# Kernel optimization log

Measured on AMD Instinct MI355X. Metric: run time of the kernel, lower is better.

The kernel has to match this reference:

```python
import jax, jax.numpy as jnp
import numpy as np

N_NODES = 100000


def setup_inputs() -> dict:
    key = jax.random.key(0)
    k1, k2, k3 = jax.random.split(key, 3)
    x = jax.random.normal(k1, (N_NODES, 64), dtype=jnp.float32)
    edge_index = jax.random.randint(k2, (2, 1250000), 0, N_NODES, dtype=jnp.int64)
    W = jax.random.normal(k3, (128, 64), dtype=jnp.float32) * (1.0 / np.sqrt(128.0))
    b = jnp.zeros((64,), dtype=jnp.float32)
    return {"x": x, "edge_index": edge_index, "W": W, "b": b}


def reference(x, edge_index, W, b):
    n = x.shape[0]
    row, col = edge_index[0], edge_index[1]
    # scatter-add neighbor features onto destination nodes
    neigh = jax.ops.segment_sum(x[row], col, num_segments=n)          # [n, d]
    count = jax.ops.segment_sum(jnp.ones_like(col, dtype=x.dtype), col, num_segments=n)
    count = jnp.where(count == 0, jnp.asarray(1.0, x.dtype), count)   # avoid div-by-zero
    neigh = neigh / count[:, None]                                    # mean aggregation
    x_aggr = jnp.concatenate([x, neigh], axis=-1)                     # [n, 2d]
    out = x_aggr @ W + b                                              # [n, out_dim]
    return jax.nn.relu(out)  # dropout=0.0 (eval) -> identity
```

## Files before the change

kernel.cpp:

```cpp
#include <hip/hip_runtime.h>

#define D 64
#define NPB 64
#define THREADS 512
#define CAP 64
#define NFILLB 1792
#define NCONVB 256

typedef int v4i __attribute__((ext_vector_type(4)));
typedef short bf16x8 __attribute__((ext_vector_type(8)));
typedef float f32x4 __attribute__((ext_vector_type(4)));

__device__ __forceinline__ unsigned short f2bf(float f) {
  unsigned u = __float_as_uint(f);
  return (unsigned short)((u + 0x7FFFu + ((u >> 16) & 1u)) >> 16);
}
__device__ __forceinline__ float bf2f(unsigned short h) {
  return __uint_as_float(((unsigned)h) << 16);
}
__device__ __forceinline__ void bfsplit(float v, unsigned short& hi, unsigned short& lo) {
  unsigned u = __float_as_uint(v);
  hi = (unsigned short)(u >> 16);
  float r = v - __uint_as_float(u & 0xFFFF0000u);
  lo = f2bf(r);
}

__global__ __launch_bounds__(256, 8) void fill_prep_kernel(
    const int* __restrict__ ei, int* __restrict__ cnt,
    int* __restrict__ bucket, int e, int qpc,
    const float* __restrict__ x, ushort* __restrict__ xh,
    const float* __restrict__ W, ushort* __restrict__ wth,
    ushort* __restrict__ wtl, int n, int total4) {
  if (blockIdx.x < NFILLB) {
    const int myx = blockIdx.x & 7;
    const int chunk = blockIdx.x >> 3;
    const int quads = e >> 2;
    const v4i* row4 = (const v4i*)ei;
    const v4i* col4 = (const v4i*)(ei + e);
    int qend = chunk * qpc + qpc;
    if (qend > quads) qend = quads;
    for (int q = chunk * qpc + threadIdx.x; q < qend; q += 256) {
      v4i r = __builtin_nontemporal_load(&row4[q]);
      v4i c = __builtin_nontemporal_load(&col4[q]);
      if (((c.x >> 11) & 7) == myx) {
        int p = atomicAdd(&cnt[c.x], 1);
        if (p < CAP) bucket[(size_t)c.x * CAP + p] = r.x * D;
      }
      if (((c.y >> 11) & 7) == myx) {
        int p = atomicAdd(&cnt[c.y], 1);
        if (p < CAP) bucket[(size_t)c.y * CAP + p] = r.y * D;
      }
      if (((c.z >> 11) & 7) == myx) {
        int p = atomicAdd(&cnt[c.z], 1);
        if (p < CAP) bucket[(size_t)c.z * CAP + p] = r.z * D;
      }
      if (((c.w >> 11) & 7) == myx) {
        int p = atomicAdd(&cnt[c.w], 1);
        if (p < CAP) bucket[(size_t)c.w * CAP + p] = r.w * D;
      }
    }
  } else {
    int t = (blockIdx.x - NFILLB) * 256 + threadIdx.x;
    int nth = NCONVB * 256;
    for (int i = t; i < 2 * D * D; i += nth) {
      int nn = i >> 7, k = i & 127;
      float v = W[k * D + nn];
      unsigned short hi, lo;
      bfsplit(v, hi, lo);
      wth[i] = hi;
      wtl[i] = lo;
    }
    for (int i = t; i < total4; i += nth) {
      float4 v = ((const float4*)x)[i];
      ushort4 h;
      h.x = f2bf(v.x); h.y = f2bf(v.y); h.z = f2bf(v.z); h.w = f2bf(v.w);
      ((ushort4*)xh)[i] = h;
    }
  }
}

__global__ __launch_bounds__(THREADS, 8) void fused_bf_kernel(
    const float* __restrict__ x, const ushort* __restrict__ xh,
    const int* __restrict__ cnt,
    const ushort* __restrict__ wth, const ushort* __restrict__ wtl,
    const float* __restrict__ b, float* __restrict__ out, int n) {
  __shared__ __align__(16) ushort xsh[NPB * 128];
  __shared__ __align__(16) ushort xsl[NPB * 128];

  const int lane = threadIdx.x & 63;
  const int wid  = threadIdx.x >> 6;
  const int base = blockIdx.x * NPB;
  const int* bucket = (const int*)out;
  const ushort* xpl = xh + lane;

  for (int m = 0; m < 8; ++m) {
    int nl = wid * 8 + m;
    int node = base + nl;
    int koff = nl * 128;
    int k0 = lane ^ ((nl & 7) << 3);
    if (node < n) {
      int dg = cnt[node];
      int dc = dg < CAP ? dg : CAP;
      int bk = bucket[(size_t)node * CAP + lane];
      float xown = x[(size_t)node * D + lane];
      float s0 = 0.f, s1 = 0.f, s2 = 0.f, s3 = 0.f;
      float s4 = 0.f, s5 = 0.f, s6 = 0.f, s7 = 0.f;
      int p = 0;
      for (; p + 8 <= dc; p += 8) {
        int a0 = __shfl(bk, p),     a1 = __shfl(bk, p + 1);
        int a2 = __shfl(bk, p + 2), a3 = __shfl(bk, p + 3);
        int a4 = __shfl(bk, p + 4), a5 = __shfl(bk, p + 5);
        int a6 = __shfl(bk, p + 6), a7 = __shfl(bk, p + 7);
        s0 += bf2f(xpl[a0]); s1 += bf2f(xpl[a1]);
        s2 += bf2f(xpl[a2]); s3 += bf2f(xpl[a3]);
        s4 += bf2f(xpl[a4]); s5 += bf2f(xpl[a5]);
        s6 += bf2f(xpl[a6]); s7 += bf2f(xpl[a7]);
      }
      for (; p + 4 <= dc; p += 4) {
        int a0 = __shfl(bk, p),     a1 = __shfl(bk, p + 1);
        int a2 = __shfl(bk, p + 2), a3 = __shfl(bk, p + 3);
        s0 += bf2f(xpl[a0]); s1 += bf2f(xpl[a1]);
        s2 += bf2f(xpl[a2]); s3 += bf2f(xpl[a3]);
      }
      for (; p < dc; ++p)
        s0 += bf2f(xpl[__shfl(bk, p)]);
      float sum = ((s0 + s1) + (s2 + s3)) + ((s4 + s5) + (s6 + s7));
      float inv = (dg > 0) ? (1.0f / (float)dg) : 0.0f;
      float mean = sum * inv;
      unsigned short h, l;
      bfsplit(xown, h, l);
      xsh[koff + k0] = h;       xsl[koff + k0] = l;
      bfsplit(mean, h, l);
      xsh[koff + 64 + k0] = h;  xsl[koff + 64 + k0] = l;
    } else {
      xsh[koff + k0] = 0;       xsl[koff + k0] = 0;
      xsh[koff + 64 + k0] = 0;  xsl[koff + 64 + k0] = 0;
    }
  }
  __syncthreads();

  const int mt   = wid >> 1;
  const int nb   = (wid & 1) * 32;
  const int lrow = lane & 15;
  const int kgrp = (lane >> 4) * 8;

  const int arow = mt * 16 + lrow;
  const int aswz = (arow & 7) << 3;
  const int abase = arow * 128;

  const ushort* wh0 = wth + (nb + lrow) * 128;
  const ushort* wh1 = wth + (nb + 16 + lrow) * 128;
  const ushort* wl0 = wtl + (nb + lrow) * 128;
  const ushort* wl1 = wtl + (nb + 16 + lrow) * 128;

  float bias0 = b[nb + lrow];
  float bias1 = b[nb + 16 + lrow];
  f32x4 acc0 = {bias0, bias0, bias0, bias0};
  f32x4 acc1 = {bias1, bias1, bias1, bias1};

#pragma unroll 2
  for (int ks = 0; ks < 4; ++ks) {
    int kb = ks * 32 + kgrp;
    int ke = abase + (kb ^ aswz);
    bf16x8 ah = *(const bf16x8*)&xsh[ke];
    bf16x8 al = *(const bf16x8*)&xsl[ke];
    bf16x8 w0h = *(const bf16x8*)(wh0 + kb);
    bf16x8 w1h = *(const bf16x8*)(wh1 + kb);
    acc0 = __builtin_amdgcn_mfma_f32_16x16x32_bf16(ah, w0h, acc0, 0, 0, 0);
    acc1 = __builtin_amdgcn_mfma_f32_16x16x32_bf16(ah, w1h, acc1, 0, 0, 0);
    acc0 = __builtin_amdgcn_mfma_f32_16x16x32_bf16(al, w0h, acc0, 0, 0, 0);
    acc1 = __builtin_amdgcn_mfma_f32_16x16x32_bf16(al, w1h, acc1, 0, 0, 0);
    bf16x8 w0l = *(const bf16x8*)(wl0 + kb);
    bf16x8 w1l = *(const bf16x8*)(wl1 + kb);
    acc0 = __builtin_amdgcn_mfma_f32_16x16x32_bf16(ah, w0l, acc0, 0, 0, 0);
    acc1 = __builtin_amdgcn_mfma_f32_16x16x32_bf16(ah, w1l, acc1, 0, 0, 0);
  }

  const int drow = (lane >> 4) * 4;
#pragma unroll
  for (int r = 0; r < 4; ++r) {
    int node = base + mt * 16 + drow + r;
    if (node < n) {
      out[(size_t)node * D + nb + lrow]      = fmaxf(acc0[r], 0.0f);
      out[(size_t)node * D + nb + 16 + lrow] = fmaxf(acc1[r], 0.0f);
    }
  }
}

__global__ __launch_bounds__(256) void fill_cap_kernel(
    const int* __restrict__ ei, int* __restrict__ cnt,
    int* __restrict__ bucket, int e) {
  int t = blockIdx.x * blockDim.x + threadIdx.x;
  if (t * 4 >= e) return;
  int4 r4 = ((const int4*)ei)[t];
  int4 c4 = ((const int4*)(ei + e))[t];
  int p0 = atomicAdd(&cnt[c4.x], 1);
  int p1 = atomicAdd(&cnt[c4.y], 1);
  int p2 = atomicAdd(&cnt[c4.z], 1);
  int p3 = atomicAdd(&cnt[c4.w], 1);
  if (p0 < CAP) bucket[(size_t)c4.x * CAP + p0] = r4.x;
  if (p1 < CAP) bucket[(size_t)c4.y * CAP + p1] = r4.y;
  if (p2 < CAP) bucket[(size_t)c4.z * CAP + p2] = r4.z;
  if (p3 < CAP) bucket[(size_t)c4.w * CAP + p3] = r4.w;
}

__global__ __launch_bounds__(THREADS, 8) void fused_cap_kernel(
    const float* __restrict__ x, const int* __restrict__ cnt,
    const float* __restrict__ W, const float* __restrict__ b,
    float* __restrict__ out, int n) {
  __shared__ __align__(16) float xs[NPB * 128];
  const int lane = threadIdx.x & 63;
  const int wid  = threadIdx.x >> 6;
  const int base = blockIdx.x * NPB;
  const int* bucket = (const int*)out;

  for (int m = 0; m < 8; ++m) {
    int nl = wid * 8 + m;
    int node = base + nl;
    if (node < n) {
      int dg = cnt[node];
      int dc = dg < CAP ? dg : CAP;
      int bk = bucket[(size_t)node * CAP + lane];
      float xown = x[(size_t)node * D + lane];
      float s0 = 0.f, s1 = 0.f, s2 = 0.f, s3 = 0.f;
      int p = 0;
      for (; p + 4 <= dc; p += 4) {
        int a0 = __shfl(bk, p),     a1 = __shfl(bk, p + 1);
        int a2 = __shfl(bk, p + 2), a3 = __shfl(bk, p + 3);
        s0 += x[(size_t)a0 * D + lane];
        s1 += x[(size_t)a1 * D + lane];
        s2 += x[(size_t)a2 * D + lane];
        s3 += x[(size_t)a3 * D + lane];
      }
      for (; p < dc; ++p)
        s0 += x[(size_t)__shfl(bk, p) * D + lane];
      float sum = (s0 + s1) + (s2 + s3);
      float inv = (dg > 0) ? (1.0f / (float)dg) : 0.0f;
      xs[nl * 128 + lane]      = xown;
      xs[nl * 128 + 64 + lane] = sum * inv;
    } else {
      xs[nl * 128 + lane]      = 0.0f;
      xs[nl * 128 + 64 + lane] = 0.0f;
    }
  }
  __syncthreads();

  const int col = lane;
  float bias = b[col];
  float acc[8];
#pragma unroll
  for (int m = 0; m < 8; ++m) acc[m] = bias;
  for (int k = 0; k < 128; k += 4) {
    float w0 = W[(k + 0) * 64 + col];
    float w1 = W[(k + 1) * 64 + col];
    float w2 = W[(k + 2) * 64 + col];
    float w3 = W[(k + 3) * 64 + col];
#pragma unroll
    for (int m = 0; m < 8; ++m) {
      int nl = wid + m * 8;
      float4 xv = *(const float4*)&xs[nl * 128 + k];
      acc[m] = fmaf(xv.x, w0, acc[m]);
      acc[m] = fmaf(xv.y, w1, acc[m]);
      acc[m] = fmaf(xv.z, w2, acc[m]);
      acc[m] = fmaf(xv.w, w3, acc[m]);
    }
  }
#pragma unroll
  for (int m = 0; m < 8; ++m) {
    int node = base + wid + m * 8;
    if (node < n)
      out[(size_t)node * D + col] = fmaxf(acc[m], 0.0f);
  }
}

extern "C" void kernel_launch(void* const* d_in, const int* in_sizes, int n_in,
                              void* d_out, int out_size, void* d_ws, size_t ws_size,
                              hipStream_t stream) {
  const float* x = (const float*)d_in[0];
  const int* ei = (const int*)d_in[1];
  const float* W = (const float*)d_in[2];
  const float* b = (const float*)d_in[3];
  float* out = (float*)d_out;

  int n = in_sizes[0] / D;
  int e = in_sizes[1] / 2;
  int nblocks = (n + NPB - 1) / NPB;

  size_t xh_bytes = (size_t)n * D * sizeof(ushort);
  size_t cnt_off  = (xh_bytes + 255) & ~(size_t)255;
  size_t wth_off  = (cnt_off + (size_t)n * sizeof(int) + 255) & ~(size_t)255;
  size_t wtl_off  = wth_off + 2 * D * D * sizeof(ushort);
  size_t need     = wtl_off + 2 * D * D * sizeof(ushort) + 256;

  if (ws_size >= need && (e & 3) == 0 && n <= (1 << 17)) {
    ushort* xh   = (ushort*)d_ws;
    int* cnt     = (int*)((char*)d_ws + cnt_off);
    ushort* wth  = (ushort*)((char*)d_ws + wth_off);
    ushort* wtl  = (ushort*)((char*)d_ws + wtl_off);

    (void)hipMemsetAsync(cnt, 0, (size_t)n * sizeof(int), stream);

    int total4 = n * D / 4;
    int quads = e >> 2;
    int chunks = NFILLB / 8;
    int qpc = (quads + chunks - 1) / chunks;

    fill_prep_kernel<<<NFILLB + NCONVB, 256, 0, stream>>>(
        ei, cnt, (int*)d_out, e, qpc, x, xh, W, wth, wtl, n, total4);

    fused_bf_kernel<<<nblocks, THREADS, 0, stream>>>(
        x, xh, cnt, wth, wtl, b, out, n);
  } else {
    int* cnt = (int*)d_ws;
    (void)hipMemsetAsync(cnt, 0, (size_t)n * sizeof(int), stream);
    int quads = e / 4;
    fill_cap_kernel<<<(quads + 255) / 256, 256, 0, stream>>>(ei, cnt, (int*)d_out, e);
    fused_cap_kernel<<<nblocks, THREADS, 0, stream>>>(x, cnt, W, b, out, n);
  }
}
```

Baseline: 202.1 us.

## Make fused kernel persistent with per-XCD atomic tile counters and lazy bucket loads

Turns the fused gather+MFMA kernel into a persistent kernel with a fixed grid of 1024 blocks. Each block pulls 64-node tiles from one of eight atomic counters, chosen by blockIdx&7, so each group of blocks works through its own interleaved stripe of tiles, which is meant to help cache locality per XCD and to balance load across uneven degrees. It also loads neighbor bucket entries for lanes 16-63 only when the node's degree exceeds 16, cutting bucket read traffic for the typical low-degree node. The costs are one atomic plus an extra barrier per tile, a larger memset that also clears the counters, and fewer resident blocks to hide gather latency.

```diff
diff --git a/kernel.cpp b/kernel.cpp
--- a/kernel.cpp
+++ b/kernel.cpp
@@ -6,6 +6,7 @@
 #define CAP 64
 #define NFILLB 1792
 #define NCONVB 256
+#define FGRID 1024
 
 typedef int v4i __attribute__((ext_vector_type(4)));
 typedef short bf16x8 __attribute__((ext_vector_type(8)));
@@ -79,110 +80,124 @@
   }
 }
 
-__global__ __launch_bounds__(THREADS, 8) void fused_bf_kernel(
+__global__ __launch_bounds__(THREADS, 8) void fused_ws_kernel(
     const float* __restrict__ x, const ushort* __restrict__ xh,
     const int* __restrict__ cnt,
     const ushort* __restrict__ wth, const ushort* __restrict__ wtl,
-    const float* __restrict__ b, float* __restrict__ out, int n) {
+    const float* __restrict__ b, float* __restrict__ out,
+    int n, int ntiles, int* __restrict__ tctr) {
   __shared__ __align__(16) ushort xsh[NPB * 128];
   __shared__ __align__(16) ushort xsl[NPB * 128];
+  __shared__ int s_tile;
 
   const int lane = threadIdx.x & 63;
   const int wid  = threadIdx.x >> 6;
-  const int base = blockIdx.x * NPB;
+  const int myx  = blockIdx.x & 7;
   const int* bucket = (const int*)out;
   const ushort* xpl = xh + lane;
-
-  for (int m = 0; m < 8; ++m) {
-    int nl = wid * 8 + m;
-    int node = base + nl;
-    int koff = nl * 128;
-    int k0 = lane ^ ((nl & 7) << 3);
-    if (node < n) {
-      int dg = cnt[node];
-      int dc = dg < CAP ? dg : CAP;
-      int bk = bucket[(size_t)node * CAP + lane];
-      float xown = x[(size_t)node * D + lane];
-      float s0 = 0.f, s1 = 0.f, s2 = 0.f, s3 = 0.f;
-      float s4 = 0.f, s5 = 0.f, s6 = 0.f, s7 = 0.f;
-      int p = 0;
-      for (; p + 8 <= dc; p += 8) {
-        int a0 = __shfl(bk, p),     a1 = __shfl(bk, p + 1);
-        int a2 = __shfl(bk, p + 2), a3 = __shfl(bk, p + 3);
-        int a4 = __shfl(bk, p + 4), a5 = __shfl(bk, p + 5);
-        int a6 = __shfl(bk, p + 6), a7 = __shfl(bk, p + 7);
-        s0 += bf2f(xpl[a0]); s1 += bf2f(xpl[a1]);
-        s2 += bf2f(xpl[a2]); s3 += bf2f(xpl[a3]);
-        s4 += bf2f(xpl[a4]); s5 += bf2f(xpl[a5]);
-        s6 += bf2f(xpl[a6]); s7 += bf2f(xpl[a7]);
-      }
-      for (; p + 4 <= dc; p += 4) {
-        int a0 = __shfl(bk, p),     a1 = __shfl(bk, p + 1);
-        int a2 = __shfl(bk, p + 2), a3 = __shfl(bk, p + 3);
-        s0 += bf2f(xpl[a0]); s1 += bf2f(xpl[a1]);
-        s2 += bf2f(xpl[a2]); s3 += bf2f(xpl[a3]);
-      }
-      for (; p < dc; ++p)
-        s0 += bf2f(xpl[__shfl(bk, p)]);
-      float sum = ((s0 + s1) + (s2 + s3)) + ((s4 + s5) + (s6 + s7));
-      float inv = (dg > 0) ? (1.0f / (float)dg) : 0.0f;
-      float mean = sum * inv;
-      unsigned short h, l;
-      bfsplit(xown, h, l);
-      xsh[koff + k0] = h;       xsl[koff + k0] = l;
-      bfsplit(mean, h, l);
-      xsh[koff + 64 + k0] = h;  xsl[koff + 64 + k0] = l;
-    } else {
-      xsh[koff + k0] = 0;       xsl[koff + k0] = 0;
-      xsh[koff + 64 + k0] = 0;  xsl[koff + 64 + k0] = 0;
-    }
-  }
-  __syncthreads();
 
   const int mt   = wid >> 1;
   const int nb   = (wid & 1) * 32;
   const int lrow = lane & 15;
   const int kgrp = (lane >> 4) * 8;
-
   const int arow = mt * 16 + lrow;
   const int aswz = (arow & 7) << 3;
   const int abase = arow * 128;
-
   const ushort* wh0 = wth + (nb + lrow) * 128;
   const ushort* wh1 = wth + (nb + 16 + lrow) * 128;
   const ushort* wl0 = wtl + (nb + lrow) * 128;
   const ushort* wl1 = wtl + (nb + 16 + lrow) * 128;
-
-  float bias0 = b[nb + lrow];
-  float bias1 = b[nb + 16 + lrow];
-  f32x4 acc0 = {bias0, bias0, bias0, bias0};
-  f32x4 acc1 = {bias1, bias1, bias1, bias1};
-
+  const float bias0 = b[nb + lrow];
+  const float bias1 = b[nb + 16 + lrow];
+  const int drow = (lane >> 4) * 4;
+
+  for (;;) {
+    if (threadIdx.x == 0) s_tile = atomicAdd(&tctr[myx * 16], 1);
+    __syncthreads();
+    const int l = s_tile;
+    const int tile = ((l >> 5) * 8 + myx) * 32 + (l & 31);
+    if (tile >= ntiles) break;
+    const int base = tile * NPB;
+
+    for (int m = 0; m < 8; ++m) {
+      int nl = wid * 8 + m;
+      int node = base + nl;
+      int koff = nl * 128;
+      int k0 = lane ^ ((nl & 7) << 3);
+      if (node < n) {
+        int dg = cnt[node];
+        int bk = 0;
+        if (lane < 16)
+          bk = bucket[(size_t)node * CAP + lane];
+        float xown = x[(size_t)node * D + lane];
+        int dc = dg < CAP ? dg : CAP;
+        if (dc > 16) {
+          if (lane >= 16)
+            bk = bucket[(size_t)node * CAP + lane];
+        }
+        float s0 = 0.f, s1 = 0.f, s2 = 0.f, s3 = 0.f;
+        float s4 = 0.f, s5 = 0.f, s6 = 0.f, s7 = 0.f;
+        int p = 0;
+        for (; p + 8 <= dc; p += 8) {
+          int a0 = __shfl(bk, p),     a1 = __shfl(bk, p + 1);
+          int a2 = __shfl(bk, p + 2), a3 = __shfl(bk, p + 3);
+          int a4 = __shfl(bk, p + 4), a5 = __shfl(bk, p + 5);
+          int a6 = __shfl(bk, p + 6), a7 = __shfl(bk, p + 7);
+          s0 += bf2f(xpl[a0]); s1 += bf2f(xpl[a1]);
+          s2 += bf2f(xpl[a2]); s3 += bf2f(xpl[a3]);
+          s4 += bf2f(xpl[a4]); s5 += bf2f(xpl[a5]);
+          s6 += bf2f(xpl[a6]); s7 += bf2f(xpl[a7]);
+        }
+        for (; p + 4 <= dc; p += 4) {
+          int a0 = __shfl(bk, p),     a1 = __shfl(bk, p + 1);
+          int a2 = __shfl(bk, p + 2), a3 = __shfl(bk, p + 3);
+          s0 += bf2f(xpl[a0]); s1 += bf2f(xpl[a1]);
+          s2 += bf2f(xpl[a2]); s3 += bf2f(xpl[a3]);
+        }
+        for (; p < dc; ++p)
+          s0 += bf2f(xpl[__shfl(bk, p)]);
+        float sum = ((s0 + s1) + (s2 + s3)) + ((s4 + s5) + (s6 + s7));
+        float inv = (dg > 0) ? (1.0f / (float)dg) : 0.0f;
+        float mean = sum * inv;
+        unsigned short h, lo;
+        bfsplit(xown, h, lo);
+        xsh[koff + k0] = h;       xsl[koff + k0] = lo;
+        bfsplit(mean, h, lo);
+        xsh[koff + 64 + k0] = h;  xsl[koff + 64 + k0] = lo;
+      } else {
+        xsh[koff + k0] = 0;       xsl[koff + k0] = 0;
+        xsh[koff + 64 + k0] = 0;  xsl[koff + 64 + k0] = 0;
+      }
+    }
+    __syncthreads();
+
+    f32x4 acc0 = {bias0, bias0, bias0, bias0};
+    f32x4 acc1 = {bias1, bias1, bias1, bias1};
 #pragma unroll 2
-  for (int ks = 0; ks < 4; ++ks) {
-    int kb = ks * 32 + kgrp;
-    int ke = abase + (kb ^ aswz);
-    bf16x8 ah = *(const bf16x8*)&xsh[ke];
-    bf16x8 al = *(const bf16x8*)&xsl[ke];
-    bf16x8 w0h = *(const bf16x8*)(wh0 + kb);
-    bf16x8 w1h = *(const bf16x8*)(wh1 + kb);
-    acc0 = __builtin_amdgcn_mfma_f32_16x16x32_bf16(ah, w0h, acc0, 0, 0, 0);
-    acc1 = __builtin_amdgcn_mfma_f32_16x16x32_bf16(ah, w1h, acc1, 0, 0, 0);
-    acc0 = __builtin_amdgcn_mfma_f32_16x16x32_bf16(al, w0h, acc0, 0, 0, 0);
-    acc1 = __builtin_amdgcn_mfma_f32_16x16x32_bf16(al, w1h, acc1, 0, 0, 0);
-    bf16x8 w0l = *(const bf16x8*)(wl0 + kb);
-    bf16x8 w1l = *(const bf16x8*)(wl1 + kb);
-    acc0 = __builtin_amdgcn_mfma_f32_16x16x32_bf16(ah, w0l, acc0, 0, 0, 0);
-    acc1 = __builtin_amdgcn_mfma_f32_16x16x32_bf16(ah, w1l, acc1, 0, 0, 0);
-  }
-
-  const int drow = (lane >> 4) * 4;
+    for (int ks = 0; ks < 4; ++ks) {
+      int kb = ks * 32 + kgrp;
+      int ke = abase + (kb ^ aswz);
+      bf16x8 ah = *(const bf16x8*)&xsh[ke];
+      bf16x8 al = *(const bf16x8*)&xsl[ke];
+      bf16x8 w0h = *(const bf16x8*)(wh0 + kb);
+      bf16x8 w1h = *(const bf16x8*)(wh1 + kb);
+      acc0 = __builtin_amdgcn_mfma_f32_16x16x32_bf16(ah, w0h, acc0, 0, 0, 0);
+      acc1 = __builtin_amdgcn_mfma_f32_16x16x32_bf16(ah, w1h, acc1, 0, 0, 0);
+      acc0 = __builtin_amdgcn_mfma_f32_16x16x32_bf16(al, w0h, acc0, 0, 0, 0);
+      acc1 = __builtin_amdgcn_mfma_f32_16x16x32_bf16(al, w1h, acc1, 0, 0, 0);
+      bf16x8 w0l = *(const bf16x8*)(wl0 + kb);
+      bf16x8 w1l = *(const bf16x8*)(wl1 + kb);
+      acc0 = __builtin_amdgcn_mfma_f32_16x16x32_bf16(ah, w0l, acc0, 0, 0, 0);
+      acc1 = __builtin_amdgcn_mfma_f32_16x16x32_bf16(ah, w1l, acc1, 0, 0, 0);
+    }
+
 #pragma unroll
-  for (int r = 0; r < 4; ++r) {
-    int node = base + mt * 16 + drow + r;
-    if (node < n) {
-      out[(size_t)node * D + nb + lrow]      = fmaxf(acc0[r], 0.0f);
-      out[(size_t)node * D + nb + 16 + lrow] = fmaxf(acc1[r], 0.0f);
+    for (int r = 0; r < 4; ++r) {
+      int node = base + mt * 16 + drow + r;
+      if (node < n) {
+        out[(size_t)node * D + nb + lrow]      = fmaxf(acc0[r], 0.0f);
+        out[(size_t)node * D + nb + 16 + lrow] = fmaxf(acc1[r], 0.0f);
+      }
     }
   }
 }
@@ -284,21 +299,23 @@
 
   int n = in_sizes[0] / D;
   int e = in_sizes[1] / 2;
-  int nblocks = (n + NPB - 1) / NPB;
+  int ntiles = (n + NPB - 1) / NPB;
 
   size_t xh_bytes = (size_t)n * D * sizeof(ushort);
   size_t cnt_off  = (xh_bytes + 255) & ~(size_t)255;
-  size_t wth_off  = (cnt_off + (size_t)n * sizeof(int) + 255) & ~(size_t)255;
+  size_t tctr_off = (cnt_off + (size_t)n * sizeof(int) + 255) & ~(size_t)255;
+  size_t wth_off  = tctr_off + 512;
   size_t wtl_off  = wth_off + 2 * D * D * sizeof(ushort);
   size_t need     = wtl_off + 2 * D * D * sizeof(ushort) + 256;
 
   if (ws_size >= need && (e & 3) == 0 && n <= (1 << 17)) {
     ushort* xh   = (ushort*)d_ws;
     int* cnt     = (int*)((char*)d_ws + cnt_off);
+    int* tctr    = (int*)((char*)d_ws + tctr_off);
     ushort* wth  = (ushort*)((char*)d_ws + wth_off);
     ushort* wtl  = (ushort*)((char*)d_ws + wtl_off);
 
-    (void)hipMemsetAsync(cnt, 0, (size_t)n * sizeof(int), stream);
+    (void)hipMemsetAsync(cnt, 0, tctr_off + 512 - cnt_off, stream);
 
     int total4 = n * D / 4;
     int quads = e >> 2;
@@ -308,13 +325,13 @@
     fill_prep_kernel<<<NFILLB + NCONVB, 256, 0, stream>>>(
         ei, cnt, (int*)d_out, e, qpc, x, xh, W, wth, wtl, n, total4);
 
-    fused_bf_kernel<<<nblocks, THREADS, 0, stream>>>(
-        x, xh, cnt, wth, wtl, b, out, n);
+    fused_ws_kernel<<<FGRID, THREADS, 0, stream>>>(
+        x, xh, cnt, wth, wtl, b, out, n, ntiles, tctr);
   } else {
     int* cnt = (int*)d_ws;
     (void)hipMemsetAsync(cnt, 0, (size_t)n * sizeof(int), stream);
     int quads = e / 4;
     fill_cap_kernel<<<(quads + 255) / 256, 256, 0, stream>>>(ei, cnt, (int*)d_out, e);
-    fused_cap_kernel<<<nblocks, THREADS, 0, stream>>>(x, cnt, W, b, out, n);
-  }
-}
+    fused_cap_kernel<<<ntiles, THREADS, 0, stream>>>(x, cnt, W, b, out, n);
+  }
+}
```

After: 206.0 us. Within noise of the previous version (+1.9%).

## Interleave two nodes' gathers and prefetch next node pair metadata

Applied to the files above, without the earlier changes.

The gather phase now processes nodes in pairs. It issues the first 8 neighbor loads of both nodes together so more memory requests are in flight per wave. It also software-prefetches the count, bucket row and own features for the next pair while the current pair is being reduced. This targets the latency of the dependent cnt→bucket→gather chain, at the cost of higher register pressure under a launch bound of 8 blocks per CU.

```diff
diff --git a/kernel.cpp b/kernel.cpp
--- a/kernel.cpp
+++ b/kernel.cpp
@@ -93,48 +93,139 @@
   const int* bucket = (const int*)out;
   const ushort* xpl = xh + lane;
 
-  for (int m = 0; m < 8; ++m) {
-    int nl = wid * 8 + m;
-    int node = base + nl;
-    int koff = nl * 128;
-    int k0 = lane ^ ((nl & 7) << 3);
-    if (node < n) {
-      int dg = cnt[node];
-      int dc = dg < CAP ? dg : CAP;
-      int bk = bucket[(size_t)node * CAP + lane];
-      float xown = x[(size_t)node * D + lane];
-      float s0 = 0.f, s1 = 0.f, s2 = 0.f, s3 = 0.f;
-      float s4 = 0.f, s5 = 0.f, s6 = 0.f, s7 = 0.f;
-      int p = 0;
-      for (; p + 8 <= dc; p += 8) {
-        int a0 = __shfl(bk, p),     a1 = __shfl(bk, p + 1);
-        int a2 = __shfl(bk, p + 2), a3 = __shfl(bk, p + 3);
-        int a4 = __shfl(bk, p + 4), a5 = __shfl(bk, p + 5);
-        int a6 = __shfl(bk, p + 6), a7 = __shfl(bk, p + 7);
-        s0 += bf2f(xpl[a0]); s1 += bf2f(xpl[a1]);
-        s2 += bf2f(xpl[a2]); s3 += bf2f(xpl[a3]);
-        s4 += bf2f(xpl[a4]); s5 += bf2f(xpl[a5]);
-        s6 += bf2f(xpl[a6]); s7 += bf2f(xpl[a7]);
-      }
-      for (; p + 4 <= dc; p += 4) {
-        int a0 = __shfl(bk, p),     a1 = __shfl(bk, p + 1);
-        int a2 = __shfl(bk, p + 2), a3 = __shfl(bk, p + 3);
-        s0 += bf2f(xpl[a0]); s1 += bf2f(xpl[a1]);
-        s2 += bf2f(xpl[a2]); s3 += bf2f(xpl[a3]);
-      }
-      for (; p < dc; ++p)
-        s0 += bf2f(xpl[__shfl(bk, p)]);
-      float sum = ((s0 + s1) + (s2 + s3)) + ((s4 + s5) + (s6 + s7));
-      float inv = (dg > 0) ? (1.0f / (float)dg) : 0.0f;
-      float mean = sum * inv;
-      unsigned short h, l;
-      bfsplit(xown, h, l);
-      xsh[koff + k0] = h;       xsl[koff + k0] = l;
-      bfsplit(mean, h, l);
-      xsh[koff + 64 + k0] = h;  xsl[koff + 64 + k0] = l;
-    } else {
-      xsh[koff + k0] = 0;       xsl[koff + k0] = 0;
-      xsh[koff + 64 + k0] = 0;  xsl[koff + 64 + k0] = 0;
+  {
+    int nA0 = base + wid * 8, nB0 = nA0 + 1;
+    int dgA = 0, bkA = 0, dgB = 0, bkB = 0;
+    float xoA = 0.f, xoB = 0.f;
+    if (nA0 < n) {
+      dgA = cnt[nA0];
+      bkA = bucket[(size_t)nA0 * CAP + lane];
+      xoA = x[(size_t)nA0 * D + lane];
+    }
+    if (nB0 < n) {
+      dgB = cnt[nB0];
+      bkB = bucket[(size_t)nB0 * CAP + lane];
+      xoB = x[(size_t)nB0 * D + lane];
+    }
+
+    for (int mm = 0; mm < 4; ++mm) {
+      const int nlA = wid * 8 + 2 * mm, nlB = nlA + 1;
+      const int nodeA = base + nlA, nodeB = base + nlB;
+      int dga = dgA, bka = bkA, dgb = dgB, bkb = bkB;
+      float xoa = xoA, xob = xoB;
+      if (mm < 3) {
+        int nA2 = nodeA + 2, nB2 = nodeB + 2;
+        if (nA2 < n) {
+          dgA = cnt[nA2];
+          bkA = bucket[(size_t)nA2 * CAP + lane];
+          xoA = x[(size_t)nA2 * D + lane];
+        } else { dgA = 0; bkA = 0; xoA = 0.f; }
+        if (nB2 < n) {
+          dgB = cnt[nB2];
+          bkB = bucket[(size_t)nB2 * CAP + lane];
+          xoB = x[(size_t)nB2 * D + lane];
+        } else { dgB = 0; bkB = 0; xoB = 0.f; }
+      }
+
+      const int dcA = dga < CAP ? dga : CAP;
+      const int dcB = dgb < CAP ? dgb : CAP;
+      float sA0 = 0.f, sA1 = 0.f, sA2 = 0.f, sA3 = 0.f;
+      float sA4 = 0.f, sA5 = 0.f, sA6 = 0.f, sA7 = 0.f;
+      float sB0 = 0.f, sB1 = 0.f, sB2 = 0.f, sB3 = 0.f;
+      float sB4 = 0.f, sB5 = 0.f, sB6 = 0.f, sB7 = 0.f;
+      int pA = 0, pB = 0;
+
+      if (nodeB < n && dcA >= 8 && dcB >= 8) {
+        int a0 = __shfl(bka, 0), a1 = __shfl(bka, 1);
+        int a2 = __shfl(bka, 2), a3 = __shfl(bka, 3);
+        int a4 = __shfl(bka, 4), a5 = __shfl(bka, 5);
+        int a6 = __shfl(bka, 6), a7 = __shfl(bka, 7);
+        int b0 = __shfl(bkb, 0), b1 = __shfl(bkb, 1);
+        int b2 = __shfl(bkb, 2), b3 = __shfl(bkb, 3);
+        int b4 = __shfl(bkb, 4), b5 = __shfl(bkb, 5);
+        int b6 = __shfl(bkb, 6), b7 = __shfl(bkb, 7);
+        ushort va0 = xpl[a0], va1 = xpl[a1], va2 = xpl[a2], va3 = xpl[a3];
+        ushort va4 = xpl[a4], va5 = xpl[a5], va6 = xpl[a6], va7 = xpl[a7];
+        ushort vb0 = xpl[b0], vb1 = xpl[b1], vb2 = xpl[b2], vb3 = xpl[b3];
+        ushort vb4 = xpl[b4], vb5 = xpl[b5], vb6 = xpl[b6], vb7 = xpl[b7];
+        sA0 += bf2f(va0); sA1 += bf2f(va1); sA2 += bf2f(va2); sA3 += bf2f(va3);
+        sA4 += bf2f(va4); sA5 += bf2f(va5); sA6 += bf2f(va6); sA7 += bf2f(va7);
+        sB0 += bf2f(vb0); sB1 += bf2f(vb1); sB2 += bf2f(vb2); sB3 += bf2f(vb3);
+        sB4 += bf2f(vb4); sB5 += bf2f(vb5); sB6 += bf2f(vb6); sB7 += bf2f(vb7);
+        pA = 8; pB = 8;
+      }
+
+      {
+        int koff = nlA * 128;
+        int k0 = lane ^ ((nlA & 7) << 3);
+        if (nodeA < n) {
+          for (; pA + 8 <= dcA; pA += 8) {
+            int a0 = __shfl(bka, pA),     a1 = __shfl(bka, pA + 1);
+            int a2 = __shfl(bka, pA + 2), a3 = __shfl(bka, pA + 3);
+            int a4 = __shfl(bka, pA + 4), a5 = __shfl(bka, pA + 5);
+            int a6 = __shfl(bka, pA + 6), a7 = __shfl(bka, pA + 7);
+            sA0 += bf2f(xpl[a0]); sA1 += bf2f(xpl[a1]);
+            sA2 += bf2f(xpl[a2]); sA3 += bf2f(xpl[a3]);
+            sA4 += bf2f(xpl[a4]); sA5 += bf2f(xpl[a5]);
+            sA6 += bf2f(xpl[a6]); sA7 += bf2f(xpl[a7]);
+          }
+          for (; pA + 4 <= dcA; pA += 4) {
+            int a0 = __shfl(bka, pA),     a1 = __shfl(bka, pA + 1);
+            int a2 = __shfl(bka, pA + 2), a3 = __shfl(bka, pA + 3);
+            sA0 += bf2f(xpl[a0]); sA1 += bf2f(xpl[a1]);
+            sA2 += bf2f(xpl[a2]); sA3 += bf2f(xpl[a3]);
+          }
+          for (; pA < dcA; ++pA)
+            sA0 += bf2f(xpl[__shfl(bka, pA)]);
+          float sum = ((sA0 + sA1) + (sA2 + sA3)) + ((sA4 + sA5) + (sA6 + sA7));
+          float inv = (dga > 0) ? (1.0f / (float)dga) : 0.0f;
+          float mean = sum * inv;
+          unsigned short h, l;
+          bfsplit(xoa, h, l);
+          xsh[koff + k0] = h;       xsl[koff + k0] = l;
+          bfsplit(mean, h, l);
+          xsh[koff + 64 + k0] = h;  xsl[koff + 64 + k0] = l;
+        } else {
+          xsh[koff + k0] = 0;       xsl[koff + k0] = 0;
+          xsh[koff + 64 + k0] = 0;  xsl[koff + 64 + k0] = 0;
+        }
+      }
+
+      {
+        int koff = nlB * 128;
+        int k0 = lane ^ ((nlB & 7) << 3);
+        if (nodeB < n) {
+          for (; pB + 8 <= dcB; pB += 8) {
+            int b0 = __shfl(bkb, pB),     b1 = __shfl(bkb, pB + 1);
+            int b2 = __shfl(bkb, pB + 2), b3 = __shfl(bkb, pB + 3);
+            int b4 = __shfl(bkb, pB + 4), b5 = __shfl(bkb, pB + 5);
+            int b6 = __shfl(bkb, pB + 6), b7 = __shfl(bkb, pB + 7);
+            sB0 += bf2f(xpl[b0]); sB1 += bf2f(xpl[b1]);
+            sB2 += bf2f(xpl[b2]); sB3 += bf2f(xpl[b3]);
+            sB4 += bf2f(xpl[b4]); sB5 += bf2f(xpl[b5]);
+            sB6 += bf2f(xpl[b6]); sB7 += bf2f(xpl[b7]);
+          }
+          for (; pB + 4 <= dcB; pB += 4) {
+            int b0 = __shfl(bkb, pB),     b1 = __shfl(bkb, pB + 1);
+            int b2 = __shfl(bkb, pB + 2), b3 = __shfl(bkb, pB + 3);
+            sB0 += bf2f(xpl[b0]); sB1 += bf2f(xpl[b1]);
+            sB2 += bf2f(xpl[b2]); sB3 += bf2f(xpl[b3]);
+          }
+          for (; pB < dcB; ++pB)
+            sB0 += bf2f(xpl[__shfl(bkb, pB)]);
+          float sum = ((sB0 + sB1) + (sB2 + sB3)) + ((sB4 + sB5) + (sB6 + sB7));
+          float inv = (dgb > 0) ? (1.0f / (float)dgb) : 0.0f;
+          float mean = sum * inv;
+          unsigned short h, l;
+          bfsplit(xob, h, l);
+          xsh[koff + k0] = h;       xsl[koff + k0] = l;
+          bfsplit(mean, h, l);
+          xsh[koff + 64 + k0] = h;  xsl[koff + 64 + k0] = l;
+        } else {
+          xsh[koff + k0] = 0;       xsl[koff + k0] = 0;
+          xsh[koff + 64 + k0] = 0;  xsl[koff + 64 + k0] = 0;
+        }
+      }
     }
   }
   __syncthreads();
```

New measurement: 207.1 us. 1.03x slower.
